# Kernel optimization log

Hardware: AMD Instinct MI355X
Metric: run time of the kernel (lower is better)

## Reference

```python
import math
import jax, jax.numpy as jnp
import numpy as np

D, NH, NL, NP = 256, 8, 3, 4
HD = D // NH
SHAPES = np.array([[92, 92], [46, 46], [23, 23]], dtype=np.int32)
LSI = np.concatenate([[0], np.cumsum(SHAPES[:, 0] * SHAPES[:, 1])[:-1]]).astype(np.int32)
LV = int((SHAPES[:, 0] * SHAPES[:, 1]).sum())  # 11109
B, LQ = 2, LV


def setup_inputs() -> dict:
    key = jax.random.key(0)
    ks = jax.random.split(key, 8)
    query = jax.random.normal(ks[0], (B, LQ, D), jnp.float32)
    reference_points = jax.random.uniform(ks[1], (B, LQ, NL, 2), dtype=jnp.float32)
    value_flat = jax.random.normal(ks[2], (B, LV, D), jnp.float32)
    # sampling_offsets: small random weight + structured directional bias (as in _reset_parameters)
    W_off = jax.random.normal(ks[3], (D, NH * NL * NP * 2), jnp.float32) * 0.01
    thetas = np.arange(NH, dtype=np.float64) * (2.0 * math.pi / NH)
    g = np.stack([np.cos(thetas), np.sin(thetas)], axis=-1)
    g = g / np.abs(g).max(axis=-1, keepdims=True)
    g = np.tile(g[:, None, None, :], (1, NL, NP, 1))
    g = g * (np.arange(NP) + 1)[None, None, :, None]
    b_off = jnp.asarray(g.reshape(-1), jnp.float32)
    W_attn = jax.random.normal(ks[4], (D, NH * NL * NP), jnp.float32) * 0.01
    b_attn = jnp.zeros((NH * NL * NP,), jnp.float32)
    W_val = jax.random.normal(ks[5], (D, D), jnp.float32) * (1.0 / math.sqrt(D))
    b_val = jnp.zeros((D,), jnp.float32)
    W_out = jax.random.normal(ks[6], (D, D), jnp.float32) * (1.0 / math.sqrt(D))
    b_out = jnp.zeros((D,), jnp.float32)
    return dict(query=query, reference_points=reference_points, value_flat=value_flat,
                W_val=W_val, b_val=b_val, W_off=W_off, b_off=b_off,
                W_attn=W_attn, b_attn=b_attn, W_out=W_out, b_out=b_out,
                spatial_shapes=jnp.asarray(SHAPES), level_start_index=jnp.asarray(LSI))


def _bilinear_sample(val_l, grid):
    """torch.F.grid_sample(mode='bilinear', padding_mode='zeros', align_corners=False).
    val_l: [B,H,W,nH,hd]; grid: [B,Q,nH,P,2] with (x,y) in [-1,1].
    Returns [B,nH,Q,P,hd]."""
    Bq, H, W, nH, hd = val_l.shape
    Q, P = grid.shape[1], grid.shape[3]
    x = ((grid[..., 0] + 1.0) * W - 1.0) * 0.5   # pixel coords, align_corners=False
    y = ((grid[..., 1] + 1.0) * H - 1.0) * 0.5
    x0f, y0f = jnp.floor(x), jnp.floor(y)
    lx, ly = x - x0f, y - y0f
    x0, y0 = x0f.astype(jnp.int32), y0f.astype(jnp.int32)
    val_bh = val_l.transpose(0, 3, 1, 2, 4).reshape(Bq * nH, H * W, hd)

    def corner(yi, xi, w):
        valid = (xi >= 0) & (xi < W) & (yi >= 0) & (yi < H)
        idx = jnp.clip(yi, 0, H - 1) * W + jnp.clip(xi, 0, W - 1)   # [B,Q,nH,P]
        idx_bh = idx.transpose(0, 2, 1, 3).reshape(Bq * nH, Q * P)
        g = jnp.take_along_axis(val_bh, idx_bh[:, :, None], axis=1)  # [B*nH, Q*P, hd]
        wm = (w * valid.astype(w.dtype)).transpose(0, 2, 1, 3).reshape(Bq * nH, Q * P, 1)
        return g * wm

    out = (corner(y0, x0, (1 - ly) * (1 - lx)) + corner(y0, x0 + 1, (1 - ly) * lx)
           + corner(y0 + 1, x0, ly * (1 - lx)) + corner(y0 + 1, x0 + 1, ly * lx))
    return out.reshape(Bq, nH, Q, P, hd)


def reference(query, reference_points, value_flat, W_val, b_val, W_off, b_off,
              W_attn, b_attn, W_out, b_out, spatial_shapes, level_start_index):
    shapes = np.asarray(spatial_shapes)          # static level geometry
    starts = np.asarray(level_start_index)
    Bq, Lq, _ = query.shape
    value = (value_flat @ W_val + b_val).reshape(Bq, -1, NH, HD)
    off = (query @ W_off + b_off).reshape(Bq, Lq, NH, NL, NP, 2)        # (dy,dx) pixels
    aw = jax.nn.softmax((query @ W_attn + b_attn).reshape(Bq, Lq, NH, NL * NP), axis=-1)
    aw = aw.reshape(Bq, Lq, NH, NL, NP)
    sh_f = jnp.asarray(shapes, jnp.float32)                              # [L,2] = (H,W)
    norm_off = off / sh_f[None, None, None, :, None, :]
    loc = reference_points[:, :, None, :, None, :] + norm_off           # [B,Lq,NH,NL,NP,2] (y,x)
    grid = 2.0 * loc[..., ::-1] - 1.0                                    # (x,y) in [-1,1]
    out = jnp.zeros((Bq, Lq, NH, HD), query.dtype)
    for l in range(NL):
        H, W = int(shapes[l, 0]), int(shapes[l, 1])
        s = int(starts[l])
        val_l = value[:, s:s + H * W].reshape(Bq, H, W, NH, HD)
        sampled = _bilinear_sample(val_l, grid[:, :, :, l])              # [B,NH,Lq,NP,HD]
        out = out + jnp.einsum('bhqpc,bqhp->bqhc', sampled, aw[:, :, :, l])
    return out.reshape(Bq, Lq, D) @ W_out + b_out
```

## Files before the change

kernel.cpp:

```cpp
#include <hip/hip_runtime.h>

#define LQn   11109
#define MTOT  22218

typedef __attribute__((ext_vector_type(8))) short short8;
typedef __attribute__((ext_vector_type(4))) float f32x4;

__device__ __forceinline__ unsigned short f2bf(float f) {
  union { float f; unsigned int u; } v; v.f = f;
  unsigned int r = v.u + 0x7fffu + ((v.u >> 16) & 1u);
  return (unsigned short)(r >> 16);
}

__global__ __launch_bounds__(256) void prep_weights(
    const float* __restrict__ Wval, const float* __restrict__ Woff,
    const float* __restrict__ Wattn, const float* __restrict__ Wout,
    const float* __restrict__ boff, const float* __restrict__ battn,
    unsigned short* __restrict__ Wval_t, unsigned short* __restrict__ Wcat_t,
    unsigned short* __restrict__ Wout_t, float* __restrict__ bcat) {
  int i = blockIdx.x * 256 + threadIdx.x;
  int n = i >> 8, k = i & 255;
  if (n < 256) {
    Wval_t[i] = f2bf(Wval[k * 256 + n]);
    Wout_t[i] = f2bf(Wout[k * 256 + n]);
  }
  float src = (n < 192) ? Woff[k * 192 + n] : Wattn[k * 96 + (n - 192)];
  Wcat_t[i] = f2bf(src);
  if (i < 288) bcat[i] = (i < 192) ? boff[i] : battn[i - 192];
}

__global__ __launch_bounds__(256) void gemm_fused12b(
    const float* __restrict__ Aval, const float* __restrict__ Aq,
    const unsigned short* __restrict__ Bval, const unsigned short* __restrict__ Bcat,
    const float* __restrict__ bval, const float* __restrict__ bcat,
    unsigned short* __restrict__ value16,
    float* __restrict__ logits) {
  __shared__ unsigned short As[64][264];
  __shared__ unsigned short Bs[64][40];

  const int bm = blockIdx.x;
  const bool is2 = blockIdx.y != 0;
  const float* __restrict__ A = is2 ? Aq : Aval;
  const unsigned short* __restrict__ Bt = is2 ? Bcat : Bval;
  const float* __restrict__ bias = is2 ? bcat : bval;
  const int N = is2 ? 288 : 256;
  const int NT = is2 ? 5 : 4;

  const int t = threadIdx.x;
  const int wave = t >> 6, lane = t & 63;
  const int wm = wave >> 1, wn = wave & 1;
  const int quad = lane >> 4, l16 = lane & 15;
  const int ldr = t >> 2;
  const int ldk = (t & 3) * 8;
  const int arow = bm * 64 + ldr;

#pragma unroll
  for (int kb = 0; kb < 8; kb++) {
    const int c0 = kb * 32 + ldk;
    float4 a0 = {0.f, 0.f, 0.f, 0.f}, a1 = a0;
    if (arow < MTOT) {
      a0 = *(const float4*)(A + (size_t)arow * 256 + c0);
      a1 = *(const float4*)(A + (size_t)arow * 256 + c0 + 4);
    }
    ushort4 lo, hi;
    lo.x = f2bf(a0.x); lo.y = f2bf(a0.y); lo.z = f2bf(a0.z); lo.w = f2bf(a0.w);
    hi.x = f2bf(a1.x); hi.y = f2bf(a1.y); hi.z = f2bf(a1.z); hi.w = f2bf(a1.w);
    *(ushort4*)(&As[ldr][c0]) = lo;
    *(ushort4*)(&As[ldr][c0 + 4]) = hi;
  }

  for (int bn = 0; bn < NT; bn++) {
    const int brow = bn * 64 + ldr;
    f32x4 acc[2][2];
    for (int i = 0; i < 2; i++)
      for (int j = 0; j < 2; j++) acc[i][j] = (f32x4){0.f, 0.f, 0.f, 0.f};

    for (int kb = 0; kb < 8; kb++) {
      uint4 bv = {0u, 0u, 0u, 0u};
      if (brow < N) bv = *(const uint4*)(Bt + (size_t)brow * 256 + kb * 32 + ldk);
      __syncthreads();
      *(uint4*)(&Bs[ldr][ldk]) = bv;
      __syncthreads();
      short8 af[2], bfr[2];
#pragma unroll
      for (int i = 0; i < 2; i++)
        af[i] = *(const short8*)(&As[wm * 32 + i * 16 + l16][kb * 32 + quad * 8]);
#pragma unroll
      for (int j = 0; j < 2; j++)
        bfr[j] = *(const short8*)(&Bs[wn * 32 + j * 16 + l16][quad * 8]);
#pragma unroll
      for (int i = 0; i < 2; i++)
#pragma unroll
        for (int j = 0; j < 2; j++)
          acc[i][j] = __builtin_amdgcn_mfma_f32_16x16x32_bf16(af[i], bfr[j], acc[i][j], 0, 0, 0);
    }

#pragma unroll
    for (int i = 0; i < 2; i++)
#pragma unroll
      for (int j = 0; j < 2; j++) {
        int colg = bn * 64 + wn * 32 + j * 16 + l16;
        if (colg >= N) continue;
        float bsv = bias[colg];
        int row0 = bm * 64 + wm * 32 + i * 16 + quad * 4;
        for (int r = 0; r < 4; r++) {
          int rg = row0 + r;
          if (rg >= MTOT) continue;
          float v = acc[i][j][r] + bsv;
          if (is2) {
            logits[(size_t)rg * 288 + colg] = v;
          } else {
            int b = (rg >= LQn) ? 1 : 0;
            int p = rg - b * LQn;
            value16[((size_t)(b * 8 + (colg >> 5)) * LQn + p) * 32 + (colg & 31)] = f2bf(v);
          }
        }
      }
  }
}

__global__ __launch_bounds__(256) void gemm_a16b(
    const unsigned short* __restrict__ A,
    const unsigned short* __restrict__ Bt,
    const float* __restrict__ bias,
    float* __restrict__ C) {
  __shared__ unsigned short As[64][264];
  __shared__ unsigned short Bs[64][40];

  const int t = threadIdx.x;
  const int bm = blockIdx.x;
  const int wave = t >> 6, lane = t & 63;
  const int wm = wave >> 1, wn = wave & 1;
  const int quad = lane >> 4, l16 = lane & 15;
  const int ldr = t >> 2;
  const int ldk = (t & 3) * 8;
  const int arow = bm * 64 + ldr;

#pragma unroll
  for (int kb = 0; kb < 8; kb++) {
    uint4 av = {0u, 0u, 0u, 0u};
    if (arow < MTOT) av = *(const uint4*)(A + (size_t)arow * 256 + kb * 32 + ldk);
    *(uint4*)(&As[ldr][kb * 32 + ldk]) = av;
  }

  for (int bn = 0; bn < 4; bn++) {
    const int brow = bn * 64 + ldr;
    f32x4 acc[2][2];
    for (int i = 0; i < 2; i++)
      for (int j = 0; j < 2; j++) acc[i][j] = (f32x4){0.f, 0.f, 0.f, 0.f};

    for (int kb = 0; kb < 8; kb++) {
      uint4 bv = *(const uint4*)(Bt + (size_t)brow * 256 + kb * 32 + ldk);
      __syncthreads();
      *(uint4*)(&Bs[ldr][ldk]) = bv;
      __syncthreads();
      short8 af[2], bfr[2];
#pragma unroll
      for (int i = 0; i < 2; i++)
        af[i] = *(const short8*)(&As[wm * 32 + i * 16 + l16][kb * 32 + quad * 8]);
#pragma unroll
      for (int j = 0; j < 2; j++)
        bfr[j] = *(const short8*)(&Bs[wn * 32 + j * 16 + l16][quad * 8]);
#pragma unroll
      for (int i = 0; i < 2; i++)
#pragma unroll
        for (int j = 0; j < 2; j++)
          acc[i][j] = __builtin_amdgcn_mfma_f32_16x16x32_bf16(af[i], bfr[j], acc[i][j], 0, 0, 0);
    }

#pragma unroll
    for (int i = 0; i < 2; i++)
#pragma unroll
      for (int j = 0; j < 2; j++) {
        int colg = bn * 64 + wn * 32 + j * 16 + l16;
        float bsv = bias[colg];
        int row0 = bm * 64 + wm * 32 + i * 16 + quad * 4;
        for (int r = 0; r < 4; r++) {
          int rg = row0 + r;
          if (rg < MTOT) C[(size_t)rg * 256 + colg] = acc[i][j][r] + bsv;
        }
      }
  }
}

__global__ __launch_bounds__(256) void msda_sample5(
    const unsigned short* __restrict__ value16,
    const float* __restrict__ logits,
    const float* __restrict__ refp,
    unsigned short* __restrict__ sampled) {
  __shared__ float          tw[8][96][4];
  __shared__ unsigned short ti[8][96][4];
  __shared__ float hmx[8][8], hrd[8][8];
  __shared__ float rfs[8][6];

  const int t = threadIdx.x;
  const int qbase = blockIdx.x * 8;

  if (t < 48) {
    int q = t / 6;
    if (qbase + q < MTOT) rfs[q][t - q * 6] = refp[(size_t)qbase * 6 + t];
  }
  if (t >= 64 && t < 128) {
    int tt = t - 64;
    int q = tt >> 3, h = tt & 7;
    int bq = qbase + q;
    if (bq < MTOT) {
      const float* lrow = logits + (size_t)bq * 288 + 192 + h * 12;
      float mx = -1e30f;
#pragma unroll
      for (int i = 0; i < 12; i++) mx = fmaxf(mx, lrow[i]);
      float den = 0.f;
#pragma unroll
      for (int i = 0; i < 12; i++) den += __expf(lrow[i] - mx);
      hmx[q][h] = mx;
      hrd[q][h] = 1.0f / den;
    }
  }
  __syncthreads();

  {
    const int Hs[3] = {92, 46, 23};
    const int Ss[3] = {0, 8464, 10580};
#pragma unroll
    for (int r = 0; r < 3; r++) {
      const int task = t + r * 256;
      const int q = task / 96, s = task - q * 96;
      const int bq = qbase + q;
      if (bq < MTOT) {
        const int h = s & 7, pl = s >> 3;
        const int l = pl >> 2;
        const int H = Hs[l], W = Hs[l], S = Ss[l];
        const int ob = h * 12 + pl;
        const float* lrow = logits + (size_t)bq * 288;
        const float aw = __expf(lrow[192 + ob] - hmx[q][h]) * hrd[q][h];
        const float offy = lrow[2 * ob], offx = lrow[2 * ob + 1];
        const float x = rfs[q][l * 2 + 1] * W + offx - 0.5f;
        const float y = rfs[q][l * 2 + 0] * H + offy - 0.5f;
        const float xf = floorf(x), yf = floorf(y);
        const int x0 = (int)xf, y0 = (int)yf;
        const float lx = x - xf, ly = y - yf;
        const bool xv0 = (x0 >= 0) & (x0 < W), xv1 = (x0 + 1 >= 0) & (x0 + 1 < W);
        const bool yv0 = (y0 >= 0) & (y0 < H), yv1 = (y0 + 1 >= 0) & (y0 + 1 < H);
        const int xc0 = min(max(x0, 0), W - 1), xc1 = min(max(x0 + 1, 0), W - 1);
        const int yc0 = min(max(y0, 0), H - 1), yc1 = min(max(y0 + 1, 0), H - 1);
        ti[q][s][0] = (unsigned short)(S + yc0 * W + xc0);
        ti[q][s][1] = (unsigned short)(S + yc0 * W + xc1);
        ti[q][s][2] = (unsigned short)(S + yc1 * W + xc0);
        ti[q][s][3] = (unsigned short)(S + yc1 * W + xc1);
        tw[q][s][0] = (yv0 & xv0) ? aw * (1.f - ly) * (1.f - lx) : 0.f;
        tw[q][s][1] = (yv0 & xv1) ? aw * (1.f - ly) * lx : 0.f;
        tw[q][s][2] = (yv1 & xv0) ? aw * ly * (1.f - lx) : 0.f;
        tw[q][s][3] = (yv1 & xv1) ? aw * ly * lx : 0.f;
      }
    }
  }
  __syncthreads();

  {
    const int w = t >> 6, lane = t & 63;
    const int q = w * 2 + (lane >> 5);
    const int h = (lane >> 2) & 7, cg = lane & 3;
    const int bq = qbase + q;
    const bool qv = bq < MTOT;
    const int bqc = qv ? bq : 0;
    const char* __restrict__ vb =
        (const char*)value16 + (size_t)(bqc / LQn) * ((size_t)LQn * 512);
    const unsigned laneoff = (unsigned)h * (LQn * 64u) + (unsigned)cg * 16u;

    float a0 = 0.f, a1 = 0.f, a2 = 0.f, a3 = 0.f;
    float a4 = 0.f, a5 = 0.f, a6 = 0.f, a7 = 0.f;
#pragma unroll
    for (int p = 0; p < 12; p++) {
      const int slot = p * 8 + h;
      const ushort4 tiv = *(const ushort4*)(&ti[q][slot][0]);
      const f32x4 wv = *(const f32x4*)(&tw[q][slot][0]);
#pragma unroll
      for (int k = 0; k < 4; k++) {
        const unsigned pix =
            (k == 0) ? tiv.x : (k == 1) ? tiv.y : (k == 2) ? tiv.z : tiv.w;
        const float wgt = wv[k];
        const uint4 u = *(const uint4*)(vb + ((pix << 6) + laneoff));
        a0 += wgt * __uint_as_float(u.x << 16);
        a1 += wgt * __uint_as_float(u.x & 0xffff0000u);
        a2 += wgt * __uint_as_float(u.y << 16);
        a3 += wgt * __uint_as_float(u.y & 0xffff0000u);
        a4 += wgt * __uint_as_float(u.z << 16);
        a5 += wgt * __uint_as_float(u.z & 0xffff0000u);
        a6 += wgt * __uint_as_float(u.w << 16);
        a7 += wgt * __uint_as_float(u.w & 0xffff0000u);
      }
    }
    if (qv) {
      uint4 o;
      o.x = (unsigned)f2bf(a0) | ((unsigned)f2bf(a1) << 16);
      o.y = (unsigned)f2bf(a2) | ((unsigned)f2bf(a3) << 16);
      o.z = (unsigned)f2bf(a4) | ((unsigned)f2bf(a5) << 16);
      o.w = (unsigned)f2bf(a6) | ((unsigned)f2bf(a7) << 16);
      *(uint4*)(sampled + (size_t)bq * 256 + h * 32 + cg * 8) = o;
    }
  }
}

extern "C" void kernel_launch(void* const* d_in, const int* in_sizes, int n_in,
                              void* d_out, int out_size, void* d_ws, size_t ws_size,
                              hipStream_t stream) {
  const float* query      = (const float*)d_in[0];
  const float* refp       = (const float*)d_in[1];
  const float* value_flat = (const float*)d_in[2];
  const float* W_val      = (const float*)d_in[3];
  const float* b_val      = (const float*)d_in[4];
  const float* W_off      = (const float*)d_in[5];
  const float* b_off      = (const float*)d_in[6];
  const float* W_attn     = (const float*)d_in[7];
  const float* b_attn     = (const float*)d_in[8];
  const float* W_out      = (const float*)d_in[9];
  const float* b_out      = (const float*)d_in[10];

  char* w = (char*)d_ws;
  size_t o = 0;
  auto carve = [&](size_t bytes) -> void* {
    void* p = (void*)(w + o);
    o += (bytes + 255) & ~(size_t)255;
    return p;
  };
  unsigned short* Wval_t  = (unsigned short*)carve(256 * 256 * 2);
  unsigned short* Wcat_t  = (unsigned short*)carve(288 * 256 * 2);
  unsigned short* Wout_t  = (unsigned short*)carve(256 * 256 * 2);
  float*          bcat    = (float*)carve(288 * 4);
  unsigned short* value16 = (unsigned short*)carve((size_t)MTOT * 256 * 2);
  float*          logits  = (float*)carve((size_t)MTOT * 288 * 4);
  unsigned short* samp_bf = (unsigned short*)carve((size_t)MTOT * 256 * 2);

  prep_weights<<<288, 256, 0, stream>>>(W_val, W_off, W_attn, W_out, b_off, b_attn,
                                        Wval_t, Wcat_t, Wout_t, bcat);

  const int mg = (MTOT + 63) / 64;
  dim3 g12(mg, 2);
  gemm_fused12b<<<g12, 256, 0, stream>>>(value_flat, query, Wval_t, Wcat_t,
                                         b_val, bcat, value16, logits);

  const int sgrid = (MTOT + 7) / 8;
  msda_sample5<<<sgrid, 256, 0, stream>>>(value16, logits, refp, samp_bf);

  gemm_a16b<<<mg, 256, 0, stream>>>(samp_bf, Wout_t, b_out, (float*)d_out);
}
```

Baseline: 194.6 us.

## Replace LDS-staged GEMMs with single-wave register-tiled MFMA tiles reading global directly

The input and output projection GEMMs drop the shared-memory staging and per-k-step barriers. Each 64-thread block now computes one 64x64 output tile, loading A and B fragments straight from global memory into registers for a 4x4 MFMA accumulator grid. The grid is split across N tiles (9 for the fused value/offset GEMM, 4 for the output GEMM), and Wcat is padded to 320 rows so no bounds checks are needed. This removes barrier overhead and the serial N loop, but A rows are re-read from global or cache once per N tile, and fp32 A is converted to bf16 again in every tile.

```diff
diff --git a/kernel.cpp b/kernel.cpp
--- a/kernel.cpp
+++ b/kernel.cpp
@@ -1,4 +1,5 @@
 #include <hip/hip_runtime.h>
+#include <hip/hip_bf16.h>
 
 #define LQn   11109
 #define MTOT  22218
@@ -12,174 +13,177 @@
   return (unsigned short)(r >> 16);
 }
 
-__global__ __launch_bounds__(256) void prep_weights(
+__device__ __forceinline__ short8 pack8(float4 a, float4 b) {
+  union { __hip_bfloat162 h[4]; short8 s; } u;
+  u.h[0] = __float22bfloat162_rn(make_float2(a.x, a.y));
+  u.h[1] = __float22bfloat162_rn(make_float2(a.z, a.w));
+  u.h[2] = __float22bfloat162_rn(make_float2(b.x, b.y));
+  u.h[3] = __float22bfloat162_rn(make_float2(b.z, b.w));
+  return u.s;
+}
+
+__global__ __launch_bounds__(320) void prep_weights2(
     const float* __restrict__ Wval, const float* __restrict__ Woff,
     const float* __restrict__ Wattn, const float* __restrict__ Wout,
     const float* __restrict__ boff, const float* __restrict__ battn,
     unsigned short* __restrict__ Wval_t, unsigned short* __restrict__ Wcat_t,
     unsigned short* __restrict__ Wout_t, float* __restrict__ bcat) {
-  int i = blockIdx.x * 256 + threadIdx.x;
-  int n = i >> 8, k = i & 255;
+  const int k = blockIdx.x;
+  const int n = threadIdx.x;
   if (n < 256) {
-    Wval_t[i] = f2bf(Wval[k * 256 + n]);
-    Wout_t[i] = f2bf(Wout[k * 256 + n]);
-  }
-  float src = (n < 192) ? Woff[k * 192 + n] : Wattn[k * 96 + (n - 192)];
-  Wcat_t[i] = f2bf(src);
-  if (i < 288) bcat[i] = (i < 192) ? boff[i] : battn[i - 192];
-}
-
-__global__ __launch_bounds__(256) void gemm_fused12b(
+    Wval_t[n * 256 + k] = f2bf(Wval[k * 256 + n]);
+    Wout_t[n * 256 + k] = f2bf(Wout[k * 256 + n]);
+  }
+  float c = (n < 192) ? Woff[k * 192 + n] : (n < 288 ? Wattn[k * 96 + (n - 192)] : 0.f);
+  Wcat_t[n * 256 + k] = f2bf(c);
+  if (k == 0) bcat[n] = (n < 192) ? boff[n] : (n < 288 ? battn[n - 192] : 0.f);
+}
+
+__global__ __launch_bounds__(64) void gemm12_tile(
     const float* __restrict__ Aval, const float* __restrict__ Aq,
     const unsigned short* __restrict__ Bval, const unsigned short* __restrict__ Bcat,
     const float* __restrict__ bval, const float* __restrict__ bcat,
     unsigned short* __restrict__ value16,
     float* __restrict__ logits) {
-  __shared__ unsigned short As[64][264];
-  __shared__ unsigned short Bs[64][40];
-
   const int bm = blockIdx.x;
-  const bool is2 = blockIdx.y != 0;
+  int bn = blockIdx.y;
+  const bool is2 = bn >= 4;
+  if (is2) bn -= 4;
   const float* __restrict__ A = is2 ? Aq : Aval;
   const unsigned short* __restrict__ Bt = is2 ? Bcat : Bval;
-  const float* __restrict__ bias = is2 ? bcat : bval;
-  const int N = is2 ? 288 : 256;
-  const int NT = is2 ? 5 : 4;
 
   const int t = threadIdx.x;
-  const int wave = t >> 6, lane = t & 63;
-  const int wm = wave >> 1, wn = wave & 1;
-  const int quad = lane >> 4, l16 = lane & 15;
-  const int ldr = t >> 2;
-  const int ldk = (t & 3) * 8;
-  const int arow = bm * 64 + ldr;
+  const int quad = t >> 4, l16 = t & 15;
+
+  const float* aptr[4];
+#pragma unroll
+  for (int i = 0; i < 4; i++) {
+    int r = bm * 64 + i * 16 + l16;
+    r = (r < MTOT) ? r : (MTOT - 1);
+    aptr[i] = A + (size_t)r * 256 + quad * 8;
+  }
+  const unsigned short* bptr[4];
+#pragma unroll
+  for (int j = 0; j < 4; j++)
+    bptr[j] = Bt + (size_t)(bn * 64 + j * 16 + l16) * 256 + quad * 8;
+
+  f32x4 acc[4][4];
+#pragma unroll
+  for (int i = 0; i < 4; i++)
+#pragma unroll
+    for (int j = 0; j < 4; j++) acc[i][j] = (f32x4){0.f, 0.f, 0.f, 0.f};
 
 #pragma unroll
   for (int kb = 0; kb < 8; kb++) {
-    const int c0 = kb * 32 + ldk;
-    float4 a0 = {0.f, 0.f, 0.f, 0.f}, a1 = a0;
-    if (arow < MTOT) {
-      a0 = *(const float4*)(A + (size_t)arow * 256 + c0);
-      a1 = *(const float4*)(A + (size_t)arow * 256 + c0 + 4);
-    }
-    ushort4 lo, hi;
-    lo.x = f2bf(a0.x); lo.y = f2bf(a0.y); lo.z = f2bf(a0.z); lo.w = f2bf(a0.w);
-    hi.x = f2bf(a1.x); hi.y = f2bf(a1.y); hi.z = f2bf(a1.z); hi.w = f2bf(a1.w);
-    *(ushort4*)(&As[ldr][c0]) = lo;
-    *(ushort4*)(&As[ldr][c0 + 4]) = hi;
-  }
-
-  for (int bn = 0; bn < NT; bn++) {
-    const int brow = bn * 64 + ldr;
-    f32x4 acc[2][2];
-    for (int i = 0; i < 2; i++)
-      for (int j = 0; j < 2; j++) acc[i][j] = (f32x4){0.f, 0.f, 0.f, 0.f};
-
-    for (int kb = 0; kb < 8; kb++) {
-      uint4 bv = {0u, 0u, 0u, 0u};
-      if (brow < N) bv = *(const uint4*)(Bt + (size_t)brow * 256 + kb * 32 + ldk);
-      __syncthreads();
-      *(uint4*)(&Bs[ldr][ldk]) = bv;
-      __syncthreads();
-      short8 af[2], bfr[2];
-#pragma unroll
-      for (int i = 0; i < 2; i++)
-        af[i] = *(const short8*)(&As[wm * 32 + i * 16 + l16][kb * 32 + quad * 8]);
-#pragma unroll
-      for (int j = 0; j < 2; j++)
-        bfr[j] = *(const short8*)(&Bs[wn * 32 + j * 16 + l16][quad * 8]);
-#pragma unroll
-      for (int i = 0; i < 2; i++)
-#pragma unroll
-        for (int j = 0; j < 2; j++)
-          acc[i][j] = __builtin_amdgcn_mfma_f32_16x16x32_bf16(af[i], bfr[j], acc[i][j], 0, 0, 0);
-    }
-
-#pragma unroll
-    for (int i = 0; i < 2; i++)
-#pragma unroll
-      for (int j = 0; j < 2; j++) {
-        int colg = bn * 64 + wn * 32 + j * 16 + l16;
-        if (colg >= N) continue;
-        float bsv = bias[colg];
-        int row0 = bm * 64 + wm * 32 + i * 16 + quad * 4;
+    short8 af[4], bfr[4];
+#pragma unroll
+    for (int i = 0; i < 4; i++) {
+      float4 a0 = *(const float4*)(aptr[i] + kb * 32);
+      float4 a1 = *(const float4*)(aptr[i] + kb * 32 + 4);
+      af[i] = pack8(a0, a1);
+    }
+#pragma unroll
+    for (int j = 0; j < 4; j++)
+      bfr[j] = *(const short8*)(bptr[j] + kb * 32);
+#pragma unroll
+    for (int i = 0; i < 4; i++)
+#pragma unroll
+      for (int j = 0; j < 4; j++)
+        acc[i][j] = __builtin_amdgcn_mfma_f32_16x16x32_bf16(af[i], bfr[j], acc[i][j], 0, 0, 0);
+  }
+
+  if (!is2) {
+#pragma unroll
+    for (int j = 0; j < 4; j++) {
+      const int col = bn * 64 + j * 16 + l16;
+      const float bs = bval[col];
+      const int h = col >> 5, cch = col & 31;
+#pragma unroll
+      for (int i = 0; i < 4; i++) {
+        const int row0 = bm * 64 + i * 16 + quad * 4;
+#pragma unroll
         for (int r = 0; r < 4; r++) {
-          int rg = row0 + r;
+          const int rg = row0 + r;
           if (rg >= MTOT) continue;
-          float v = acc[i][j][r] + bsv;
-          if (is2) {
-            logits[(size_t)rg * 288 + colg] = v;
-          } else {
-            int b = (rg >= LQn) ? 1 : 0;
-            int p = rg - b * LQn;
-            value16[((size_t)(b * 8 + (colg >> 5)) * LQn + p) * 32 + (colg & 31)] = f2bf(v);
-          }
+          const int b = (rg >= LQn) ? 1 : 0;
+          const int p = rg - b * LQn;
+          value16[((size_t)(b * 8 + h) * LQn + p) * 32 + cch] = f2bf(acc[i][j][r] + bs);
         }
       }
-  }
-}
-
-__global__ __launch_bounds__(256) void gemm_a16b(
+    }
+  } else {
+#pragma unroll
+    for (int j = 0; j < 4; j++) {
+      const int col = bn * 64 + j * 16 + l16;
+      if (col >= 288) continue;
+      const float bs = bcat[col];
+#pragma unroll
+      for (int i = 0; i < 4; i++) {
+        const int row0 = bm * 64 + i * 16 + quad * 4;
+#pragma unroll
+        for (int r = 0; r < 4; r++) {
+          const int rg = row0 + r;
+          if (rg < MTOT) logits[(size_t)rg * 288 + col] = acc[i][j][r] + bs;
+        }
+      }
+    }
+  }
+}
+
+__global__ __launch_bounds__(64) void gemm_out_tile(
     const unsigned short* __restrict__ A,
     const unsigned short* __restrict__ Bt,
     const float* __restrict__ bias,
     float* __restrict__ C) {
-  __shared__ unsigned short As[64][264];
-  __shared__ unsigned short Bs[64][40];
-
+  const int bm = blockIdx.x, bn = blockIdx.y;
   const int t = threadIdx.x;
-  const int bm = blockIdx.x;
-  const int wave = t >> 6, lane = t & 63;
-  const int wm = wave >> 1, wn = wave & 1;
-  const int quad = lane >> 4, l16 = lane & 15;
-  const int ldr = t >> 2;
-  const int ldk = (t & 3) * 8;
-  const int arow = bm * 64 + ldr;
+  const int quad = t >> 4, l16 = t & 15;
+
+  const unsigned short* aptr[4];
+#pragma unroll
+  for (int i = 0; i < 4; i++) {
+    int r = bm * 64 + i * 16 + l16;
+    r = (r < MTOT) ? r : (MTOT - 1);
+    aptr[i] = A + (size_t)r * 256 + quad * 8;
+  }
+  const unsigned short* bptr[4];
+#pragma unroll
+  for (int j = 0; j < 4; j++)
+    bptr[j] = Bt + (size_t)(bn * 64 + j * 16 + l16) * 256 + quad * 8;
+
+  f32x4 acc[4][4];
+#pragma unroll
+  for (int i = 0; i < 4; i++)
+#pragma unroll
+    for (int j = 0; j < 4; j++) acc[i][j] = (f32x4){0.f, 0.f, 0.f, 0.f};
 
 #pragma unroll
   for (int kb = 0; kb < 8; kb++) {
-    uint4 av = {0u, 0u, 0u, 0u};
-    if (arow < MTOT) av = *(const uint4*)(A + (size_t)arow * 256 + kb * 32 + ldk);
-    *(uint4*)(&As[ldr][kb * 32 + ldk]) = av;
-  }
-
-  for (int bn = 0; bn < 4; bn++) {
-    const int brow = bn * 64 + ldr;
-    f32x4 acc[2][2];
-    for (int i = 0; i < 2; i++)
-      for (int j = 0; j < 2; j++) acc[i][j] = (f32x4){0.f, 0.f, 0.f, 0.f};
-
-    for (int kb = 0; kb < 8; kb++) {
-      uint4 bv = *(const uint4*)(Bt + (size_t)brow * 256 + kb * 32 + ldk);
-      __syncthreads();
-      *(uint4*)(&Bs[ldr][ldk]) = bv;
-      __syncthreads();
-      short8 af[2], bfr[2];
-#pragma unroll
-      for (int i = 0; i < 2; i++)
-        af[i] = *(const short8*)(&As[wm * 32 + i * 16 + l16][kb * 32 + quad * 8]);
-#pragma unroll
-      for (int j = 0; j < 2; j++)
-        bfr[j] = *(const short8*)(&Bs[wn * 32 + j * 16 + l16][quad * 8]);
-#pragma unroll
-      for (int i = 0; i < 2; i++)
-#pragma unroll
-        for (int j = 0; j < 2; j++)
-          acc[i][j] = __builtin_amdgcn_mfma_f32_16x16x32_bf16(af[i], bfr[j], acc[i][j], 0, 0, 0);
-    }
-
-#pragma unroll
-    for (int i = 0; i < 2; i++)
-#pragma unroll
-      for (int j = 0; j < 2; j++) {
-        int colg = bn * 64 + wn * 32 + j * 16 + l16;
-        float bsv = bias[colg];
-        int row0 = bm * 64 + wm * 32 + i * 16 + quad * 4;
-        for (int r = 0; r < 4; r++) {
-          int rg = row0 + r;
-          if (rg < MTOT) C[(size_t)rg * 256 + colg] = acc[i][j][r] + bsv;
-        }
-      }
+    short8 af[4], bfr[4];
+#pragma unroll
+    for (int i = 0; i < 4; i++) af[i] = *(const short8*)(aptr[i] + kb * 32);
+#pragma unroll
+    for (int j = 0; j < 4; j++) bfr[j] = *(const short8*)(bptr[j] + kb * 32);
+#pragma unroll
+    for (int i = 0; i < 4; i++)
+#pragma unroll
+      for (int j = 0; j < 4; j++)
+        acc[i][j] = __builtin_amdgcn_mfma_f32_16x16x32_bf16(af[i], bfr[j], acc[i][j], 0, 0, 0);
+  }
+
+#pragma unroll
+  for (int j = 0; j < 4; j++) {
+    const int col = bn * 64 + j * 16 + l16;
+    const float bs = bias[col];
+#pragma unroll
+    for (int i = 0; i < 4; i++) {
+      const int row0 = bm * 64 + i * 16 + quad * 4;
+#pragma unroll
+      for (int r = 0; r < 4; r++) {
+        const int rg = row0 + r;
+        if (rg < MTOT) C[(size_t)rg * 256 + col] = acc[i][j][r] + bs;
+      }
+    }
   }
 }
 
@@ -324,23 +328,24 @@
     return p;
   };
   unsigned short* Wval_t  = (unsigned short*)carve(256 * 256 * 2);
-  unsigned short* Wcat_t  = (unsigned short*)carve(288 * 256 * 2);
+  unsigned short* Wcat_t  = (unsigned short*)carve(320 * 256 * 2);
   unsigned short* Wout_t  = (unsigned short*)carve(256 * 256 * 2);
-  float*          bcat    = (float*)carve(288 * 4);
+  float*          bcat    = (float*)carve(320 * 4);
   unsigned short* value16 = (unsigned short*)carve((size_t)MTOT * 256 * 2);
   float*          logits  = (float*)carve((size_t)MTOT * 288 * 4);
   unsigned short* samp_bf = (unsigned short*)carve((size_t)MTOT * 256 * 2);
 
-  prep_weights<<<288, 256, 0, stream>>>(W_val, W_off, W_attn, W_out, b_off, b_attn,
-                                        Wval_t, Wcat_t, Wout_t, bcat);
+  prep_weights2<<<256, 320, 0, stream>>>(W_val, W_off, W_attn, W_out, b_off, b_attn,
+                                         Wval_t, Wcat_t, Wout_t, bcat);
 
   const int mg = (MTOT + 63) / 64;
-  dim3 g12(mg, 2);
-  gemm_fused12b<<<g12, 256, 0, stream>>>(value_flat, query, Wval_t, Wcat_t,
-                                         b_val, bcat, value16, logits);
+  dim3 g12(mg, 9);
+  gemm12_tile<<<g12, 64, 0, stream>>>(value_flat, query, Wval_t, Wcat_t,
+                                      b_val, bcat, value16, logits);
 
   const int sgrid = (MTOT + 7) / 8;
   msda_sample5<<<sgrid, 256, 0, stream>>>(value16, logits, refp, samp_bf);
 
-  gemm_a16b<<<mg, 256, 0, stream>>>(samp_bf, Wout_t, b_out, (float*)d_out);
-}
+  dim3 g3(mg, 4);
+  gemm_out_tile<<<g3, 64, 0, stream>>>(samp_bf, Wout_t, b_out, (float*)d_out);
+}
```

New measurement: 224.1 us. 1.15x slower.
